# Kernel optimization log

Measured on AMD Instinct MI355X. Metric: run time of the kernel, lower is better.

Reference implementation:

```python
import jax, jax.numpy as jnp
import numpy as np

C = 256
H = W = 80
PATCH = 3  # patchsize, stride 1 -> npatches = (H-2)*(W-2) = 6084


def setup_inputs() -> dict:
    key = jax.random.key(0)
    k_style, k_x = jax.random.split(key)
    style = jax.random.normal(k_style, (1, C, H, W), jnp.float32)
    # torch: activation.unfold(2,3,1).unfold(3,3,1).squeeze() -> (C, nH, nW, 3, 3)
    #        .permute(1,2,0,3,4).view(nH*nW, C, 3, 3)
    s = np.asarray(style)
    win = np.lib.stride_tricks.sliding_window_view(s, (PATCH, PATCH), axis=(2, 3))  # (1,C,78,78,3,3)
    patches = np.ascontiguousarray(win[0].transpose(1, 2, 0, 3, 4).reshape(-1, C, PATCH, PATCH))
    x = jax.random.normal(k_x, (1, C, H, W), jnp.float32)
    return {"x": x, "patches": jnp.asarray(patches)}


def reference(x, patches):
    # NOTE: the original's per-patch normalization uses .mul (not .mul_), a no-op,
    # so conv_enc weight == raw patches, same as conv_dec. Replicated here.
    npatches = patches.shape[0]
    dn = ("NCHW", "OIHW", "NCHW")
    # conv_enc: valid 3x3 conv, patches as filters -> (1, npatches, 78, 78)
    sim = jax.lax.conv_general_dilated(x, patches, (1, 1), "VALID", dimension_numbers=dn)
    # per-pixel argmax over patch channel + one-hot (replaces the python double loop)
    idx = jnp.argmax(sim, axis=1)  # (1, 78, 78)
    onehot = jax.nn.one_hot(idx, npatches, axis=1, dtype=x.dtype)  # (1, npatches, 78, 78)
    # conv_dec / aux: ConvTranspose2d == adjoint of the valid conv (transpose_kernel=True)
    swap = jax.lax.conv_transpose(onehot, patches, (1, 1), "VALID", dimension_numbers=dn, transpose_kernel=True)
    swap_wei = jax.lax.conv_transpose(onehot, jnp.ones_like(patches), (1, 1), "VALID", dimension_numbers=dn, transpose_kernel=True)
    return swap / swap_wei  # (1, C, 80, 80)
```

## Files before the change

kernel.cpp:

```cpp
#include <hip/hip_runtime.h>
#include <stdint.h>

#define NPIX 6084
#define NPAD 6144
#define KDIM 2304
#define KB   (KDIM*2)
#define NT   36

typedef __attribute__((ext_vector_type(8))) short s16x8;
typedef __attribute__((ext_vector_type(4))) float f32x4;

__device__ __forceinline__ short f2bf(float f) {
  unsigned u = __builtin_bit_cast(unsigned, f);
  u += 0x7FFFu + ((u >> 16) & 1u);
  return (short)(u >> 16);
}
__device__ __forceinline__ float bf2f(short s) {
  unsigned u = ((unsigned)(unsigned short)s) << 16;
  return __builtin_bit_cast(float, u);
}

#define GL16(g, l)                                                            \
  __builtin_amdgcn_global_load_lds(                                           \
      (__attribute__((address_space(1))) unsigned int*)(g),                   \
      (__attribute__((address_space(3))) unsigned int*)(l), 16, 0, 0)

__global__ __launch_bounds__(256) void k_prep_pat(const float* __restrict__ pat,
                                                  short* __restrict__ out) {
  int i = blockIdx.x * 256 + threadIdx.x;
  int e0 = i * 8;
  int row = e0 / KDIM;
  s16x8 v;
  if (row < NPIX) {
    const float* s = pat + e0;
#pragma unroll
    for (int j = 0; j < 8; ++j) v[j] = f2bf(s[j]);
  } else {
#pragma unroll
    for (int j = 0; j < 8; ++j) v[j] = 0;
  }
  *(s16x8*)(out + e0) = v;
}

__global__ __launch_bounds__(256) void k_xcol2(const float* __restrict__ x,
                                               short* __restrict__ out) {
  __shared__ float lx[7680];
  const int b = blockIdx.x, tid = threadIdx.x;
  if (b >= 624) {
    int i = b - 624;
    s16x8 z = {};
#pragma unroll
    for (int it = 0; it < 9; ++it) {
      int t = i * 2160 + it * 256 + tid;
      if (t < 17280) ((s16x8*)out)[(size_t)NPIX * KDIM / 8 + t] = z;
    }
    return;
  }
  const int p = b >> 3, cc = b & 7;
  for (int t = tid; t < 7680; t += 256) {
    int ci = t / 240, rr = t - ci * 240;
    lx[t] = x[(cc * 32 + ci) * 6400 + p * 80 + rr];
  }
  __syncthreads();
  for (int t = tid; t < 22464; t += 256) {
    int q = t / 288, e = t - q * 288;
    int ci = e / 9, r = e - ci * 9;
    int dy = r / 3, dx = r - dy * 3;
    out[(size_t)(p * 78 + q) * KDIM + cc * 288 + e] =
        f2bf(lx[ci * 240 + dy * 80 + q + dx]);
  }
}

__global__ __launch_bounds__(512, 2) void k_gemm(const short* __restrict__ A,
                                                 const short* __restrict__ B,
                                                 short* __restrict__ C) {
  __shared__ __align__(1024) char smem[131072];
  const int tid = threadIdx.x;
  const int w = tid >> 6, lane = tid & 63;
  const int wr = w >> 2, wc = w & 3;
  const int tm = blockIdx.y, tn = blockIdx.x;
  const char* Ab = (const char*)A + (size_t)tm * 256 * KB;
  const char* Bb = (const char*)B + (size_t)tn * 256 * KB;

  const int srccol = ((lane & 7) * 16) ^ ((lane >> 3) << 4);
  const int lrow = lane >> 3;
  const int fragRow = lane & 15;
  const int swz = (lane & 7) << 4;
  const int colb0 = (lane >> 4) * 16;
  const int aOff = (wr * 128 + fragRow) * 128;
  const int bOff = 32768 + (wc * 64 + fragRow) * 128;

  f32x4 acc[8][4] = {};
  s16x8 a[4][2];
  s16x8 b[2][2][2];

#define STAGE_A(par, hs, kt)                                                  \
  _Pragma("unroll") for (int j = 0; j < 2; ++j) {                             \
    int c = w * 2 + j;                                                        \
    int rb = (c < 8) ? (hs)*64 + c * 8 : 128 + (hs)*64 + (c - 8) * 8;         \
    GL16(Ab + (size_t)(rb + lrow) * KB + (kt)*128 + srccol,                   \
         smem + (par)*65536 + rb * 128);                                      \
  }
#define STAGE_B(par, hs, kt)                                                  \
  _Pragma("unroll") for (int j = 0; j < 2; ++j) {                             \
    int c = w * 2 + j;                                                        \
    int rb = (c >> 2) * 64 + (hs)*32 + (c & 3) * 8;                           \
    GL16(Bb + (size_t)(rb + lrow) * KB + (kt)*128 + srccol,                   \
         smem + (par)*65536 + 32768 + rb * 128);                              \
  }
#define LDA(par, mh)                                                          \
  _Pragma("unroll") for (int mi2 = 0; mi2 < 4; ++mi2)                         \
  _Pragma("unroll") for (int ks = 0; ks < 2; ++ks)                            \
    a[mi2][ks] = *(const s16x8*)(smem + (par)*65536 + aOff + (mh)*8192 +      \
                                 mi2 * 2048 + ((colb0 + ks * 64) ^ swz));
#define LDB(par, nh)                                                          \
  _Pragma("unroll") for (int ni2 = 0; ni2 < 2; ++ni2)                         \
  _Pragma("unroll") for (int ks = 0; ks < 2; ++ks)                            \
    b[nh][ni2][ks] = *(const s16x8*)(smem + (par)*65536 + bOff + (nh)*4096 +  \
                                     ni2 * 2048 + ((colb0 + ks * 64) ^ swz));
#define VM6() asm volatile("s_waitcnt vmcnt(6)" ::: "memory")
#define BAR() asm volatile("s_barrier" ::: "memory")
#define BARL() asm volatile("s_barrier\n\ts_waitcnt lgkmcnt(0)" ::: "memory")
#define QM(mh, nh)                                                            \
  do {                                                                        \
    __builtin_amdgcn_s_setprio(1);                                            \
    _Pragma("unroll") for (int mi2 = 0; mi2 < 4; ++mi2)                       \
    _Pragma("unroll") for (int ni2 = 0; ni2 < 2; ++ni2)                       \
    _Pragma("unroll") for (int ks = 0; ks < 2; ++ks)                          \
      acc[(mh)*4 + mi2][(nh)*2 + ni2] =                                       \
          __builtin_amdgcn_mfma_f32_16x16x32_bf16(                            \
              a[mi2][ks], b[nh][ni2][ks], acc[(mh)*4 + mi2][(nh)*2 + ni2],    \
              0, 0, 0);                                                       \
    __builtin_amdgcn_s_setprio(0);                                            \
    BAR();                                                                    \
  } while (0)

  STAGE_A(0, 0, 0); STAGE_B(0, 0, 0); STAGE_B(0, 1, 0); STAGE_A(0, 1, 0);
  STAGE_A(1, 0, 1); STAGE_B(1, 0, 1); STAGE_B(1, 1, 1);
  VM6();
  BAR();

#pragma unroll 1
  for (int i = 0; i < NT / 2; ++i) {
    const int t2 = (2 * i + 2 < NT) ? 2 * i + 2 : NT - 1;
    const int t3 = (2 * i + 3 < NT) ? 2 * i + 3 : NT - 1;
    LDA(0, 0); LDB(0, 0);
    STAGE_A(1, 1, 2 * i + 1);
    BARL(); QM(0, 0);
    LDB(0, 1);
    STAGE_A(0, 0, t2);
    BARL(); QM(0, 1);
    LDA(0, 1);
    STAGE_B(0, 0, t2);
    BARL(); QM(1, 1);
    STAGE_B(0, 1, t2);
    VM6();
    BARL(); QM(1, 0);
    LDA(1, 0); LDB(1, 0);
    STAGE_A(0, 1, t2);
    BARL(); QM(0, 0);
    LDB(1, 1);
    STAGE_A(1, 0, t3);
    BARL(); QM(0, 1);
    LDA(1, 1);
    STAGE_B(1, 0, t3);
    BARL(); QM(1, 1);
    STAGE_B(1, 1, t3);
    VM6();
    BARL(); QM(1, 0);
  }

  const int rowb = tm * 256 + wr * 128 + (lane >> 4) * 4;
  const int colb = tn * 256 + wc * 64 + (lane & 15);
#pragma unroll
  for (int mi = 0; mi < 8; ++mi)
#pragma unroll
    for (int ni = 0; ni < 4; ++ni)
#pragma unroll
      for (int j = 0; j < 4; ++j)
        C[(size_t)(rowb + mi * 16 + j) * NPAD + colb + ni * 16] =
            f2bf(acc[mi][ni][j]);
}

__global__ __launch_bounds__(256) void k_rowmax(const short* __restrict__ sim,
                                                float* __restrict__ gval,
                                                int* __restrict__ gidx) {
  const int tid = threadIdx.x, w = tid >> 6, lane = tid & 63;
  const int row = blockIdx.x * 4 + w;
  const short* r = sim + (size_t)row * NPAD;
#pragma unroll 1
  for (int p = 0; p < 12; ++p) {
    int c0 = p * 512 + lane * 8;
    s16x8 v = *(const s16x8*)(r + c0);
    float bv = -1e30f;
    int bc = 0x7FFFFFFF;
#pragma unroll
    for (int j = 0; j < 8; ++j) {
      int k = c0 + j;
      float f = bf2f(v[j]);
      if (k < NPIX && (f > bv || (f == bv && k < bc))) { bv = f; bc = k; }
    }
#pragma unroll
    for (int off = 1; off < 32; off <<= 1) {
      float ov = __shfl_xor(bv, off);
      int oc = __shfl_xor(bc, off);
      if (ov > bv || (ov == bv && oc < bc)) { bv = ov; bc = oc; }
    }
    if ((lane & 31) == 0) {
      int seg = p * 2 + (lane >> 5);
      gval[seg * NPAD + row] = bv;
      gidx[seg * NPAD + row] = bc;
    }
  }
}

__global__ __launch_bounds__(256) void k_argmax2(const short* __restrict__ sim,
                                                 const float* __restrict__ gval,
                                                 const int* __restrict__ gidx,
                                                 const float* __restrict__ x,
                                                 const float* __restrict__ pat,
                                                 int* __restrict__ amax) {
  __shared__ int cand[4][32];
  __shared__ int ccnt[4];
  const int tid = threadIdx.x, w = tid >> 6, lane = tid & 63;
  const int pix = blockIdx.x * 4 + w;

  float v0 = (lane < 24) ? gval[lane * NPAD + pix] : -1e30f;
  int c0 = (lane < 24) ? gidx[lane * NPAD + pix] : 0x7FFFFFFF;
  float v = v0;
  int c = c0;
  for (int off = 32; off; off >>= 1) {
    float ov = __shfl_down(v, off);
    int oc = __shfl_down(c, off);
    if (ov > v || (ov == v && oc < c)) { v = ov; c = oc; }
  }
  const float maxv = __shfl(v, 0);
  const int bestc = __shfl(c, 0);

  if (lane == 0) ccnt[w] = 0;
  __syncthreads();

  const float thrb = maxv - 4.0f;
  for (int t = 0; t < 24; ++t) {
    float bm = __shfl(v0, t);
    if (bm >= thrb) {
      short4 s4 = *(const short4*)(sim + (size_t)pix * NPAD + t * 256 + lane * 4);
#pragma unroll
      for (int j = 0; j < 4; ++j) {
        int k = t * 256 + lane * 4 + j;
        float f = bf2f(((const short*)&s4)[j]);
        if (f >= thrb - 0.6f && k < NPIX) {
          int pos = atomicAdd(&ccnt[w], 1);
          if (pos < 32) cand[w][pos] = k;
        }
      }
    }
  }
  __syncthreads();

  int n = ccnt[w] < 32 ? ccnt[w] : 32;
  if (n <= 1) {
    if (lane == 0) amax[pix] = bestc;
    return;
  }
  const int p = pix / 78, q = pix - (pix / 78) * 78;
  double bests = -1e300;
  int bestk = 0;
  for (int ci = 0; ci < n; ++ci) {
    int k = cand[w][ci];
    double s = 0.0;
    for (int cc = lane; cc < 256; cc += 64) {
      const float* xb = x + cc * 6400 + p * 80 + q;
      const float* pb = pat + (size_t)k * KDIM + cc * 9;
#pragma unroll
      for (int dy = 0; dy < 3; ++dy)
#pragma unroll
        for (int dx = 0; dx < 3; ++dx)
          s += (double)xb[dy * 80 + dx] * (double)pb[dy * 3 + dx];
    }
    for (int off = 32; off; off >>= 1) s += __shfl_down(s, off);
    if (lane == 0 && (s > bests || (s == bests && k < bestk))) {
      bests = s; bestk = k;
    }
  }
  if (lane == 0) amax[pix] = bestk;
}

__global__ __launch_bounds__(256) void k_scat9(const float* __restrict__ pat,
                                               const int* __restrict__ amax,
                                               float* __restrict__ plane) {
  __shared__ float lp[KDIM];
  const int b = blockIdx.x;
  const int k = amax[b];
  const int p = b / 78, q = b - (b / 78) * 78;
  const float* src = pat + (size_t)k * KDIM;
#pragma unroll
  for (int j = 0; j < 9; ++j) lp[j * 256 + threadIdx.x] = src[j * 256 + threadIdx.x];
  __syncthreads();
  const int c = threadIdx.x;
#pragma unroll
  for (int r = 0; r < 9; ++r) {
    int dy = r / 3, dx = r - dy * 3;
    int pos = (p + dy) * 80 + (q + dx);
    plane[(size_t)r * 1638400 + pos * 256 + c] = lp[c * 9 + r];
  }
}

__global__ __launch_bounds__(256) void k_reduce(const float* __restrict__ plane,
                                                float* __restrict__ out) {
  const int c = threadIdx.x;
  const int pix0 = blockIdx.x * 16;
  for (int i = 0; i < 16; ++i) {
    int pix = pix0 + i;
    int yy = pix / 80, xx = pix - (pix / 80) * 80;
    float s = 0.f;
    int cnt = 0;
#pragma unroll
    for (int r = 0; r < 9; ++r) {
      int dy = r / 3, dx = r - dy * 3;
      int p = yy - dy, q = xx - dx;
      if (p >= 0 && p < 78 && q >= 0 && q < 78) {
        s += plane[(size_t)r * 1638400 + pix * 256 + c];
        ++cnt;
      }
    }
    out[c * 6400 + pix] = s / (float)cnt;
  }
}

extern "C" void kernel_launch(void* const* d_in, const int* in_sizes, int n_in,
                              void* d_out, int out_size, void* d_ws,
                              size_t ws_size, hipStream_t stream) {
  const float* x = (const float*)d_in[0];
  const float* pat = (const float*)d_in[1];
  float* out = (float*)d_out;
  char* ws = (char*)d_ws;

  short* patB = (short*)ws;
  short* xcol = (short*)(ws + 28311552);
  short* sim  = (short*)(ws + 2 * 28311552);
  float* plane = (float*)sim;
  int*   amax = (int*)(ws + 132120576);
  float* gval = (float*)(ws + 132144912);
  int*   gidx = (int*)(ws + 132734736);

  k_prep_pat<<<6912, 256, 0, stream>>>(pat, patB);
  k_xcol2<<<632, 256, 0, stream>>>(x, xcol);
  k_gemm<<<dim3(24, 24), 512, 0, stream>>>(xcol, patB, sim);
  k_rowmax<<<1521, 256, 0, stream>>>(sim, gval, gidx);
  k_argmax2<<<1521, 256, 0, stream>>>(sim, gval, gidx, x, pat, amax);
  k_scat9<<<6084, 256, 0, stream>>>(pat, amax, plane);
  k_reduce<<<400, 256, 0, stream>>>(plane, out);
}
```

Before: 420.0 us.

## Fuse prep kernels and row argmax passes, store scatter plane in bf16

Merges the patch conversion and im2col kernels into one launch, and fuses the row-max and candidate-refinement kernels so per-segment maxima stay in shared memory instead of global buffers. The scatter plane used for overlap averaging is stored as bf16 instead of fp32, halving that large intermediate's write and read traffic. The candidate threshold margin is tightened, which may drop near-tie candidates, and bf16 storage of patch values adds rounding to the output.

```diff
diff --git a/kernel.cpp b/kernel.cpp
--- a/kernel.cpp
+++ b/kernel.cpp
@@ -25,38 +25,39 @@
       (__attribute__((address_space(1))) unsigned int*)(g),                   \
       (__attribute__((address_space(3))) unsigned int*)(l), 16, 0, 0)
 
-__global__ __launch_bounds__(256) void k_prep_pat(const float* __restrict__ pat,
-                                                  short* __restrict__ out) {
-  int i = blockIdx.x * 256 + threadIdx.x;
-  int e0 = i * 8;
-  int row = e0 / KDIM;
-  s16x8 v;
-  if (row < NPIX) {
-    const float* s = pat + e0;
-#pragma unroll
-    for (int j = 0; j < 8; ++j) v[j] = f2bf(s[j]);
-  } else {
-#pragma unroll
-    for (int j = 0; j < 8; ++j) v[j] = 0;
-  }
-  *(s16x8*)(out + e0) = v;
-}
-
-__global__ __launch_bounds__(256) void k_xcol2(const float* __restrict__ x,
-                                               short* __restrict__ out) {
+__global__ __launch_bounds__(256) void k_prep(const float* __restrict__ pat,
+                                              const float* __restrict__ x,
+                                              short* __restrict__ patB,
+                                              short* __restrict__ xcol) {
   __shared__ float lx[7680];
   const int b = blockIdx.x, tid = threadIdx.x;
-  if (b >= 624) {
-    int i = b - 624;
+  if (b < 6912) {
+    int e0 = (b * 256 + tid) * 8;
+    int row = e0 / KDIM;
+    s16x8 v;
+    if (row < NPIX) {
+      const float* s = pat + e0;
+#pragma unroll
+      for (int j = 0; j < 8; ++j) v[j] = f2bf(s[j]);
+    } else {
+#pragma unroll
+      for (int j = 0; j < 8; ++j) v[j] = 0;
+    }
+    *(s16x8*)(patB + e0) = v;
+    return;
+  }
+  const int bb = b - 6912;
+  if (bb >= 624) {
+    int i = bb - 624;
     s16x8 z = {};
 #pragma unroll
     for (int it = 0; it < 9; ++it) {
       int t = i * 2160 + it * 256 + tid;
-      if (t < 17280) ((s16x8*)out)[(size_t)NPIX * KDIM / 8 + t] = z;
+      if (t < 17280) ((s16x8*)xcol)[(size_t)NPIX * KDIM / 8 + t] = z;
     }
     return;
   }
-  const int p = b >> 3, cc = b & 7;
+  const int p = bb >> 3, cc = bb & 7;
   for (int t = tid; t < 7680; t += 256) {
     int ci = t / 240, rr = t - ci * 240;
     lx[t] = x[(cc * 32 + ci) * 6400 + p * 80 + rr];
@@ -66,7 +67,7 @@
     int q = t / 288, e = t - q * 288;
     int ci = e / 9, r = e - ci * 9;
     int dy = r / 3, dx = r - dy * 3;
-    out[(size_t)(p * 78 + q) * KDIM + cc * 288 + e] =
+    xcol[(size_t)(p * 78 + q) * KDIM + cc * 288 + e] =
         f2bf(lx[ci * 240 + dy * 80 + q + dx]);
   }
 }
@@ -182,74 +183,61 @@
             f2bf(acc[mi][ni][j]);
 }
 
-__global__ __launch_bounds__(256) void k_rowmax(const short* __restrict__ sim,
-                                                float* __restrict__ gval,
-                                                int* __restrict__ gidx) {
-  const int tid = threadIdx.x, w = tid >> 6, lane = tid & 63;
-  const int row = blockIdx.x * 4 + w;
-  const short* r = sim + (size_t)row * NPAD;
-#pragma unroll 1
-  for (int p = 0; p < 12; ++p) {
-    int c0 = p * 512 + lane * 8;
-    s16x8 v = *(const s16x8*)(r + c0);
-    float bv = -1e30f;
-    int bc = 0x7FFFFFFF;
-#pragma unroll
-    for (int j = 0; j < 8; ++j) {
-      int k = c0 + j;
-      float f = bf2f(v[j]);
-      if (k < NPIX && (f > bv || (f == bv && k < bc))) { bv = f; bc = k; }
-    }
-#pragma unroll
-    for (int off = 1; off < 32; off <<= 1) {
-      float ov = __shfl_xor(bv, off);
-      int oc = __shfl_xor(bc, off);
-      if (ov > bv || (ov == bv && oc < bc)) { bv = ov; bc = oc; }
-    }
-    if ((lane & 31) == 0) {
-      int seg = p * 2 + (lane >> 5);
-      gval[seg * NPAD + row] = bv;
-      gidx[seg * NPAD + row] = bc;
-    }
-  }
-}
-
-__global__ __launch_bounds__(256) void k_argmax2(const short* __restrict__ sim,
-                                                 const float* __restrict__ gval,
-                                                 const int* __restrict__ gidx,
-                                                 const float* __restrict__ x,
-                                                 const float* __restrict__ pat,
-                                                 int* __restrict__ amax) {
+__global__ __launch_bounds__(256) void k_rowargmax(const short* __restrict__ sim,
+                                                   const float* __restrict__ x,
+                                                   const float* __restrict__ pat,
+                                                   int* __restrict__ amax) {
+  __shared__ float segmax[4][24];
   __shared__ int cand[4][32];
   __shared__ int ccnt[4];
   const int tid = threadIdx.x, w = tid >> 6, lane = tid & 63;
   const int pix = blockIdx.x * 4 + w;
-
-  float v0 = (lane < 24) ? gval[lane * NPAD + pix] : -1e30f;
-  int c0 = (lane < 24) ? gidx[lane * NPAD + pix] : 0x7FFFFFFF;
-  float v = v0;
-  int c = c0;
-  for (int off = 32; off; off >>= 1) {
-    float ov = __shfl_down(v, off);
-    int oc = __shfl_down(c, off);
-    if (ov > v || (ov == v && oc < c)) { v = ov; c = oc; }
-  }
-  const float maxv = __shfl(v, 0);
-  const int bestc = __shfl(c, 0);
+  const short* row = sim + (size_t)pix * NPAD;
+
+  float bv = -1e30f;
+  int bc = 0x7FFFFFFF;
+#pragma unroll 1
+  for (int p = 0; p < 12; ++p) {
+    int c0 = p * 512 + lane * 8;
+    s16x8 v = *(const s16x8*)(row + c0);
+    float sb = -1e30f;
+    int sc = 0x7FFFFFFF;
+#pragma unroll
+    for (int j = 0; j < 8; ++j) {
+      int k = c0 + j;
+      float f = bf2f(v[j]);
+      if (k < NPIX && (f > sb || (f == sb && k < sc))) { sb = f; sc = k; }
+    }
+    if (sb > bv || (sb == bv && sc < bc)) { bv = sb; bc = sc; }
+#pragma unroll
+    for (int off = 1; off < 32; off <<= 1) {
+      float ov = __shfl_xor(sb, off);
+      if (ov > sb) sb = ov;
+    }
+    if ((lane & 31) == 0) segmax[w][p * 2 + (lane >> 5)] = sb;
+  }
+#pragma unroll
+  for (int off = 1; off < 64; off <<= 1) {
+    float ov = __shfl_xor(bv, off);
+    int oc = __shfl_xor(bc, off);
+    if (ov > bv || (ov == bv && oc < bc)) { bv = ov; bc = oc; }
+  }
+  const float maxv = bv;
+  const int bestc = bc;
 
   if (lane == 0) ccnt[w] = 0;
   __syncthreads();
 
-  const float thrb = maxv - 4.0f;
-  for (int t = 0; t < 24; ++t) {
-    float bm = __shfl(v0, t);
-    if (bm >= thrb) {
-      short4 s4 = *(const short4*)(sim + (size_t)pix * NPAD + t * 256 + lane * 4);
+  const float thr = maxv - 4.0f;
+#pragma unroll 1
+  for (int seg = 0; seg < 24; ++seg) {
+    if (segmax[w][seg] >= thr) {
+      short4 s4 = *(const short4*)(row + seg * 256 + lane * 4);
 #pragma unroll
       for (int j = 0; j < 4; ++j) {
-        int k = t * 256 + lane * 4 + j;
+        int k = seg * 256 + lane * 4 + j;
         float f = bf2f(((const short*)&s4)[j]);
-        if (f >= thrb - 0.6f && k < NPIX) {
+        if (f >= thr && k < NPIX) {
           int pos = atomicAdd(&ccnt[w], 1);
           if (pos < 32) cand[w][pos] = k;
         }
@@ -288,7 +276,7 @@
 
 __global__ __launch_bounds__(256) void k_scat9(const float* __restrict__ pat,
                                                const int* __restrict__ amax,
-                                               float* __restrict__ plane) {
+                                               short* __restrict__ plane) {
   __shared__ float lp[KDIM];
   const int b = blockIdx.x;
   const int k = amax[b];
@@ -302,11 +290,11 @@
   for (int r = 0; r < 9; ++r) {
     int dy = r / 3, dx = r - dy * 3;
     int pos = (p + dy) * 80 + (q + dx);
-    plane[(size_t)r * 1638400 + pos * 256 + c] = lp[c * 9 + r];
-  }
-}
-
-__global__ __launch_bounds__(256) void k_reduce(const float* __restrict__ plane,
+    plane[(size_t)r * 1638400 + pos * 256 + c] = f2bf(lp[c * 9 + r]);
+  }
+}
+
+__global__ __launch_bounds__(256) void k_reduce(const short* __restrict__ plane,
                                                 float* __restrict__ out) {
   const int c = threadIdx.x;
   const int pix0 = blockIdx.x * 16;
@@ -320,7 +308,7 @@
       int dy = r / 3, dx = r - dy * 3;
       int p = yy - dy, q = xx - dx;
       if (p >= 0 && p < 78 && q >= 0 && q < 78) {
-        s += plane[(size_t)r * 1638400 + pix * 256 + c];
+        s += bf2f(plane[(size_t)r * 1638400 + pix * 256 + c]);
         ++cnt;
       }
     }
@@ -339,16 +327,12 @@
   short* patB = (short*)ws;
   short* xcol = (short*)(ws + 28311552);
   short* sim  = (short*)(ws + 2 * 28311552);
-  float* plane = (float*)sim;
+  short* plane = sim;
   int*   amax = (int*)(ws + 132120576);
-  float* gval = (float*)(ws + 132144912);
-  int*   gidx = (int*)(ws + 132734736);
-
-  k_prep_pat<<<6912, 256, 0, stream>>>(pat, patB);
-  k_xcol2<<<632, 256, 0, stream>>>(x, xcol);
+
+  k_prep<<<7544, 256, 0, stream>>>(pat, x, patB, xcol);
   k_gemm<<<dim3(24, 24), 512, 0, stream>>>(xcol, patB, sim);
-  k_rowmax<<<1521, 256, 0, stream>>>(sim, gval, gidx);
-  k_argmax2<<<1521, 256, 0, stream>>>(sim, gval, gidx, x, pat, amax);
+  k_rowargmax<<<1521, 256, 0, stream>>>(sim, x, pat, amax);
   k_scat9<<<6084, 256, 0, stream>>>(pat, amax, plane);
   k_reduce<<<400, 256, 0, stream>>>(plane, out);
 }
```

After: 403.5 us. 3.9% less time.
